# Optimization experiments

Hardware: AMD Instinct MI355X
Metric: run time of the kernel (lower is better)

Reference implementation:

```python
import jax, jax.numpy as jnp
import numpy as np

N_EMBD = 512
N_HEAD = 8
HEAD_DIM = N_EMBD // N_HEAD
MAX_REL = 5
B, T = 8, 1024  # T must be <= 2*N_EMBD due to scores[:, :, :T, :T] slice


def setup_inputs() -> dict:
    key = jax.random.key(0)
    ks = jax.random.split(key, 10)
    C, d = N_EMBD, HEAD_DIM
    s = 1.0 / np.sqrt(C)
    return {
        "x": jax.random.normal(ks[0], (B, T, C), jnp.float32),
        # nn.Linear weights are [out, in]
        "w1_w": jax.random.normal(ks[1], (C, C), jnp.float32) * s,
        "w1_b": jnp.zeros((C,), jnp.float32),
        "w2": jax.random.uniform(ks[2], (d, 2 * C), jnp.float32, -0.001, 0.001),
        "b2": jnp.zeros((2 * C,), jnp.float32),
        "v_w": jax.random.normal(ks[3], (C, C), jnp.float32) * s,
        "v_b": jnp.zeros((C,), jnp.float32),
        "proj_w": jax.random.normal(ks[4], (C, C), jnp.float32) * s,
        "proj_b": jnp.zeros((C,), jnp.float32),
        # RelativePosition embeddings table: [2*max_rel+1, head_dim]
        "rel_v_table": jax.random.normal(ks[5], (2 * MAX_REL + 1, d), jnp.float32) * s,
    }


def reference(x, w1_w, w1_b, w2, b2, v_w, v_b, proj_w, proj_b, rel_v_table):
    Bq, Tq, C = x.shape
    H, d = N_HEAD, C // N_HEAD
    # per-position MLP synthesizer scores: relu(w1(x)) [B,H,T,d] @ w2 [d,2C] + b2
    relu_out = jax.nn.relu(x @ w1_w.T + w1_b).reshape(Bq, Tq, H, d).transpose(0, 2, 1, 3)
    scores = (relu_out @ w2 + b2)[:, :, :, :Tq]  # [B,H,T,T]
    causal = jnp.tril(jnp.ones((Tq, Tq), dtype=bool))
    scores = jnp.where(causal[None, None], scores, jnp.float32(-1e10))
    prob_attn = jax.nn.softmax(scores, axis=-1)
    # standard value path
    v = (x @ v_w.T + v_b).reshape(Bq, Tq, H, d).transpose(0, 2, 1, 3)  # [B,H,T,d]
    y1 = prob_attn @ v  # [B,H,T,d]
    # relative-position value path: table lookup per (q,k) pair
    dist = jnp.arange(Tq)[None, :] - jnp.arange(Tq)[:, None]
    idx = jnp.clip(dist, -MAX_REL, 0) + MAX_REL  # [T,T] in [0, 2*MAX_REL]
    v2 = rel_v_table[idx]  # [T,T,d]
    y2 = jnp.einsum('bhqk,qkd->bhqd', prob_attn, v2)
    y = (y1 + y2).transpose(0, 2, 1, 3).reshape(Bq, Tq, C)
    return y @ proj_w.T + proj_b
```

## Files before the change

kernel.cpp:

```cpp
#include <hip/hip_runtime.h>
#include <cstdint>

#define B_ 8
#define T_ 1024
#define C_ 512
#define H_ 8

typedef __attribute__((ext_vector_type(8))) short bf16x8;
typedef __attribute__((ext_vector_type(4))) float f32x4;

__device__ __forceinline__ unsigned short f2bf(float f) {
  uint32_t u = __float_as_uint(f);
  u += 0x7FFFu + ((u >> 16) & 1u);
  return (unsigned short)(u >> 16);
}
__device__ __forceinline__ float bf2f(unsigned short h) {
  return __uint_as_float(((uint32_t)h) << 16);
}

__global__ __launch_bounds__(256) void cvt_bf16(
    const float* __restrict__ in, unsigned short* __restrict__ out, int n4) {
  int i = blockIdx.x * 256 + threadIdx.x;
  if (i < n4) {
    float4 f = reinterpret_cast<const float4*>(in)[i];
    uint2 o;
    o.x = (uint32_t)f2bf(f.x) | ((uint32_t)f2bf(f.y) << 16);
    o.y = (uint32_t)f2bf(f.z) | ((uint32_t)f2bf(f.w) << 16);
    reinterpret_cast<uint2*>(out)[i] = o;
  }
}

__global__ __launch_bounds__(256) void transpose_cvt(
    const float* __restrict__ in, unsigned short* __restrict__ out, int R, int Cc) {
  __shared__ float tile[32][33];
  const int c0 = blockIdx.x * 32, r0 = blockIdx.y * 32;
  const int t = threadIdx.x;
  {
    int ri = t >> 3, ci = (t & 7) * 4;
    float4 f = *reinterpret_cast<const float4*>(&in[(size_t)(r0 + ri) * Cc + c0 + ci]);
    tile[ri][ci] = f.x; tile[ri][ci + 1] = f.y; tile[ri][ci + 2] = f.z; tile[ri][ci + 3] = f.w;
  }
  __syncthreads();
  {
    int co = t >> 3, ro = (t & 7) * 4;
    uint2 o;
    o.x = (uint32_t)f2bf(tile[ro][co])     | ((uint32_t)f2bf(tile[ro + 1][co]) << 16);
    o.y = (uint32_t)f2bf(tile[ro + 2][co]) | ((uint32_t)f2bf(tile[ro + 3][co]) << 16);
    *reinterpret_cast<uint2*>(&out[(size_t)(c0 + co) * R + r0 + ro]) = o;
  }
}

__global__ __launch_bounds__(256) void transpose_bb(
    const unsigned short* __restrict__ in, unsigned short* __restrict__ out, int R, int Cc) {
  __shared__ unsigned short tile[32][36];
  const int c0 = blockIdx.x * 32, r0 = blockIdx.y * 32;
  const int t = threadIdx.x;
  {
    int ri = t >> 3, ci = (t & 7) * 4;
    uint2 d = *reinterpret_cast<const uint2*>(&in[(size_t)(r0 + ri) * Cc + c0 + ci]);
    *reinterpret_cast<uint2*>(&tile[ri][ci]) = d;
  }
  __syncthreads();
  {
    int co = t >> 3, ro = (t & 7) * 4;
    uint2 o;
    o.x = (uint32_t)tile[ro][co]     | ((uint32_t)tile[ro + 1][co] << 16);
    o.y = (uint32_t)tile[ro + 2][co] | ((uint32_t)tile[ro + 3][co] << 16);
    *reinterpret_cast<uint2*>(&out[(size_t)(c0 + co) * R + r0 + ro]) = o;
  }
}

template<bool RELU, bool OBF16>
__global__ __launch_bounds__(256) void gemm_mfma(
    const unsigned short* __restrict__ A, const unsigned short* __restrict__ W,
    const float* __restrict__ bias, void* __restrict__ out,
    int M, int N, int K)
{
  __shared__ unsigned short As[128 * 64];
  __shared__ unsigned short Ws[128 * 64];

  const int tid = threadIdx.x;
  const int lane = tid & 63;
  const int wid = tid >> 6;
  const int wm = wid >> 1, wn = wid & 1;
  const int m0 = blockIdx.y * 128, n0 = blockIdx.x * 128;
  const int r15 = lane & 15, g4 = lane >> 4;

  f32x4 acc[4][4] = {};

  for (int k0 = 0; k0 < K; k0 += 64) {
    __syncthreads();
    #pragma unroll
    for (int p = 0; p < 4; ++p) {
      int idx = tid + p * 256;
      int row = idx >> 3, sl = idx & 7;
      int byte = row * 128 + sl * 16;
      byte ^= ((byte >> 9) & 1) << 5;
      uint4 da = *reinterpret_cast<const uint4*>(&A[(size_t)(m0 + row) * K + k0 + sl * 8]);
      *reinterpret_cast<uint4*>(reinterpret_cast<char*>(As) + byte) = da;
      uint4 dw = *reinterpret_cast<const uint4*>(&W[(size_t)(n0 + row) * K + k0 + sl * 8]);
      *reinterpret_cast<uint4*>(reinterpret_cast<char*>(Ws) + byte) = dw;
    }
    __syncthreads();
    #pragma unroll
    for (int ks = 0; ks < 2; ++ks) {
      bf16x8 af[4], bfr[4];
      #pragma unroll
      for (int f = 0; f < 4; ++f) {
        int ab = (wm * 64 + f * 16 + r15) * 128 + ks * 64 + g4 * 16;
        ab ^= ((ab >> 9) & 1) << 5;
        af[f] = *reinterpret_cast<const bf16x8*>(reinterpret_cast<char*>(As) + ab);
        int bb = (wn * 64 + f * 16 + r15) * 128 + ks * 64 + g4 * 16;
        bb ^= ((bb >> 9) & 1) << 5;
        bfr[f] = *reinterpret_cast<const bf16x8*>(reinterpret_cast<char*>(Ws) + bb);
      }
      #pragma unroll
      for (int i = 0; i < 4; ++i)
        #pragma unroll
        for (int j = 0; j < 4; ++j)
          acc[i][j] = __builtin_amdgcn_mfma_f32_16x16x32_bf16(af[i], bfr[j], acc[i][j], 0, 0, 0);
    }
  }

  #pragma unroll
  for (int i = 0; i < 4; ++i) {
    int m = m0 + wm * 64 + i * 16 + g4 * 4;
    #pragma unroll
    for (int j = 0; j < 4; ++j) {
      int n = n0 + wn * 64 + j * 16 + r15;
      float bj = bias[n];
      #pragma unroll
      for (int rg = 0; rg < 4; ++rg) {
        float z = acc[i][j][rg] + bj;
        z = RELU ? fmaxf(z, 0.f) : z;
        if (OBF16) ((unsigned short*)out)[(size_t)(m + rg) * N + n] = f2bf(z);
        else       ((float*)out)[(size_t)(m + rg) * N + n] = z;
      }
    }
  }
}

#define SA_VLOAD(K0)                                                                  \
  do {                                                                                \
    { int c = tid;       int row = c >> 3, sl = c & 7;                                \
      w0 = *reinterpret_cast<const uint4*>(&w2t[(size_t)((K0) + row) * 64 + sl * 8]); } \
    { int c = tid + 256; int row = c >> 3, sl = c & 7;                                \
      w1 = *reinterpret_cast<const uint4*>(&w2t[(size_t)((K0) + row) * 64 + sl * 8]); } \
    { int c = tid;       int row = c >> 3, sl = c & 7;                                \
      v0 = *reinterpret_cast<const uint4*>(&vT[(size_t)(h * 64 + row) * 8192 + b * 1024 + (K0) + sl * 8]); } \
    { int c = tid + 256; int row = c >> 3, sl = c & 7;                                \
      v1 = *reinterpret_cast<const uint4*>(&vT[(size_t)(h * 64 + row) * 8192 + b * 1024 + (K0) + sl * 8]); } \
    if (tid < 16) bq = *reinterpret_cast<const float4*>(&b2[(K0) + tid * 4]);         \
  } while (0)

#define SA_VSTORE()                                                                   \
  do {                                                                                \
    { int c = tid;       int row = c >> 3, sl = c & 7;                                \
      *reinterpret_cast<uint4*>(W2 + row * 128 + ((sl ^ (row & 7)) << 4)) = w0; }     \
    { int c = tid + 256; int row = c >> 3, sl = c & 7;                                \
      *reinterpret_cast<uint4*>(W2 + row * 128 + ((sl ^ (row & 7)) << 4)) = w1; }     \
    { int c = tid;       int row = c >> 3, sl = c & 7;                                \
      *reinterpret_cast<uint4*>(Vt + row * 128 + ((sl ^ (row & 7)) << 4)) = v0; }     \
    { int c = tid + 256; int row = c >> 3, sl = c & 7;                                \
      *reinterpret_cast<uint4*>(Vt + row * 128 + ((sl ^ (row & 7)) << 4)) = v1; }     \
    if (tid < 16) *reinterpret_cast<float4*>(&b2L[tid * 4]) = bq;                     \
  } while (0)

__global__ __launch_bounds__(256) void synth_attn_mfma(
    const unsigned short* __restrict__ rb, const unsigned short* __restrict__ vT,
    const unsigned short* __restrict__ w2t, const float* __restrict__ b2,
    const float* __restrict__ table, unsigned short* __restrict__ ya)
{
  __shared__ alignas(16) unsigned short RtS[64 * 64];
  __shared__ alignas(16) unsigned short W2S[64 * 64];
  __shared__ alignas(16) unsigned short ElS[64 * 64];
  __shared__ alignas(16) unsigned short VtS[80 * 64];
  __shared__ float b2L[64];
  __shared__ float tap[64][5];
  __shared__ float tabs[6][64];

  char* Rt = (char*)RtS;
  char* W2 = (char*)W2S;
  char* El = (char*)ElS;
  char* Vt = (char*)VtS;

  const int tid = threadIdx.x;
  const int lane = tid & 63, w = tid >> 6;
  const int l15 = lane & 15, g = lane >> 4;
  const int bid = blockIdx.x;
  const int pp = bid & 7;
  const int bh = bid >> 3;
  const int b = bh >> 3, h = bh & 7;

  #pragma unroll
  for (int t2 = 0; t2 < 2; ++t2) {
    int idx = tid + t2 * 256;
    if (idx < 384) ((float*)tabs)[idx] = table[idx];
  }
  {
    int row = 64 + (tid >> 4), chunk = tid & 15;
    uint2 val;
    val.x = (row == 64) ? 0x3F803F80u : 0u;
    val.y = val.x;
    *reinterpret_cast<uint2*>(Vt + row * 128 + chunk * 8) = val;
  }

  uint4 w0, w1, v0, v1; float4 bq;

  for (int half = 0; half < 2; ++half) {
    const int qt = half ? (15 - pp) : pp;
    const int q0 = qt * 64;

    __syncthreads();
    #pragma unroll
    for (int t2 = 0; t2 < 2; ++t2) {
      int c = tid + t2 * 256; int row = c >> 3, sl = c & 7;
      uint4 d = *reinterpret_cast<const uint4*>(
          &rb[(size_t)(b * 1024 + q0 + row) * 512 + h * 64 + sl * 8]);
      *reinterpret_cast<uint4*>(Rt + row * 128 + ((sl ^ (row & 7)) << 4)) = d;
    }
    if (lane < 16) {
      int qr = w * 16 + lane;
      #pragma unroll
      for (int jj = 0; jj < 5; ++jj) tap[qr][jj] = 0.f;
    }

    f32x4 acc[4] = {};
    f32x4 accS = {};

    SA_VLOAD(0);
    for (int kt = 0; kt <= qt; ++kt) {
      const int k0 = kt * 64;
      __syncthreads();
      SA_VSTORE();
      if (kt < qt) SA_VLOAD(k0 + 64);
      __syncthreads();

      const int arow = w * 16 + l15;
      const int arx = l15 & 7;
      bf16x8 a0 = *reinterpret_cast<const bf16x8*>(Rt + arow * 128 + ((g ^ arx) << 4));
      bf16x8 a1 = *reinterpret_cast<const bf16x8*>(Rt + arow * 128 + (((4 + g) ^ arx) << 4));
      f32x4 sf[4] = {};
      #pragma unroll
      for (int j = 0; j < 4; ++j) {
        int row = 16 * j + l15, rx = row & 7;
        bf16x8 b0 = *reinterpret_cast<const bf16x8*>(W2 + row * 128 + ((g ^ rx) << 4));
        bf16x8 b1 = *reinterpret_cast<const bf16x8*>(W2 + row * 128 + (((4 + g) ^ rx) << 4));
        sf[j] = __builtin_amdgcn_mfma_f32_16x16x32_bf16(a0, b0, sf[j], 0, 0, 0);
        sf[j] = __builtin_amdgcn_mfma_f32_16x16x32_bf16(a1, b1, sf[j], 0, 0, 0);
      }

      if (kt == qt) {
        #pragma unroll
        for (int j = 0; j < 4; ++j) {
          int kc = 16 * j + l15;
          float bk = b2L[kc];
          #pragma unroll
          for (int rr = 0; rr < 4; ++rr) {
            int qr = w * 16 + g * 4 + rr;
            float ex = (kc <= qr) ? __expf(sf[j][rr] + bk) : 0.f;
            int byte = qr * 128 + ((((kc >> 3) ^ (qr & 7)) << 4) | ((kc & 7) << 1));
            *reinterpret_cast<unsigned short*>(El + byte) = f2bf(ex);
          }
        }
      } else {
        #pragma unroll
        for (int j = 0; j < 4; ++j) {
          int kc = 16 * j + l15;
          float bk = b2L[kc];
          #pragma unroll
          for (int rr = 0; rr < 4; ++rr) {
            int qr = w * 16 + g * 4 + rr;
            float ex = __expf(sf[j][rr] + bk);
            int byte = qr * 128 + ((((kc >> 3) ^ (qr & 7)) << 4) | ((kc & 7) << 1));
            *reinterpret_cast<unsigned short*>(El + byte) = f2bf(ex);
          }
        }
      }

      bf16x8 ae0 = *reinterpret_cast<const bf16x8*>(El + arow * 128 + ((g ^ arx) << 4));
      bf16x8 ae1 = *reinterpret_cast<const bf16x8*>(El + arow * 128 + (((4 + g) ^ arx) << 4));
      #pragma unroll
      for (int j = 0; j < 4; ++j) {
        int row = 16 * j + l15, rx = row & 7;
        bf16x8 vb0 = *reinterpret_cast<const bf16x8*>(Vt + row * 128 + ((g ^ rx) << 4));
        bf16x8 vb1 = *reinterpret_cast<const bf16x8*>(Vt + row * 128 + (((4 + g) ^ rx) << 4));
        acc[j] = __builtin_amdgcn_mfma_f32_16x16x32_bf16(ae0, vb0, acc[j], 0, 0, 0);
        acc[j] = __builtin_amdgcn_mfma_f32_16x16x32_bf16(ae1, vb1, acc[j], 0, 0, 0);
      }
      {
        int row = 64 + l15, rx = row & 7;
        bf16x8 o0 = *reinterpret_cast<const bf16x8*>(Vt + row * 128 + ((g ^ rx) << 4));
        bf16x8 o1 = *reinterpret_cast<const bf16x8*>(Vt + row * 128 + (((4 + g) ^ rx) << 4));
        accS = __builtin_amdgcn_mfma_f32_16x16x32_bf16(ae0, o0, accS, 0, 0, 0);
        accS = __builtin_amdgcn_mfma_f32_16x16x32_bf16(ae1, o1, accS, 0, 0, 0);
      }

      if (lane < 16) {
        int qr = w * 16 + lane;
        int off = q0 + qr - 4 - k0;
        #pragma unroll
        for (int jj = 0; jj < 5; ++jj) {
          int kk = off + jj;
          if ((unsigned)kk < 64u) {
            int byte = qr * 128 + ((((kk >> 3) ^ (qr & 7)) << 4) | ((kk & 7) << 1));
            tap[qr][jj] += bf2f(*reinterpret_cast<unsigned short*>(El + byte));
          }
        }
      }
    }

    float inv[4], tp[4][5];
    #pragma unroll
    for (int rr = 0; rr < 4; ++rr) {
      float ls = __shfl(accS[rr], lane & 48, 64);
      inv[rr] = 1.f / ls;
      int qr = w * 16 + g * 4 + rr;
      #pragma unroll
      for (int jj = 0; jj < 5; ++jj) tp[rr][jj] = tap[qr][jj] * inv[rr];
    }
    #pragma unroll
    for (int j = 0; j < 4; ++j) {
      int dd = 16 * j + l15;
      float t0 = tabs[0][dd];
      float dt[5];
      #pragma unroll
      for (int jj = 0; jj < 5; ++jj) dt[jj] = tabs[jj + 1][dd] - t0;
      #pragma unroll
      for (int rr = 0; rr < 4; ++rr) {
        int qr = w * 16 + g * 4 + rr;
        float y = acc[j][rr] * inv[rr] + t0;
        #pragma unroll
        for (int jj = 0; jj < 5; ++jj) y = fmaf(tp[rr][jj], dt[jj], y);
        ya[(size_t)(b * 1024 + q0 + qr) * 512 + h * 64 + dd] = f2bf(y);
      }
    }
  }
}

extern "C" void kernel_launch(void* const* d_in, const int* in_sizes, int n_in,
                              void* d_out, int out_size, void* d_ws, size_t ws_size,
                              hipStream_t stream) {
  const float* x      = (const float*)d_in[0];
  const float* w1_w   = (const float*)d_in[1];
  const float* w1_b   = (const float*)d_in[2];
  const float* w2     = (const float*)d_in[3];
  const float* b2     = (const float*)d_in[4];
  const float* v_w    = (const float*)d_in[5];
  const float* v_b    = (const float*)d_in[6];
  const float* proj_w = (const float*)d_in[7];
  const float* proj_b = (const float*)d_in[8];
  const float* relv   = (const float*)d_in[9];
  float* out = (float*)d_out;

  const size_t buf = (size_t)B_ * T_ * C_;
  const size_t wsz = (size_t)C_ * C_;
  unsigned short* rb    = (unsigned short*)d_ws;
  unsigned short* vbb   = rb + buf;
  unsigned short* xb    = vbb + buf;
  unsigned short* w1b   = xb + buf;
  unsigned short* vwb   = w1b + wsz;
  unsigned short* projb = vwb + wsz;
  unsigned short* w2t   = projb + wsz;
  unsigned short* vT    = xb;
  unsigned short* yab   = vbb;

  cvt_bf16<<<(int)(buf / 4 + 255) / 256, 256, 0, stream>>>(x, xb, (int)(buf / 4));
  cvt_bf16<<<(int)(wsz / 4 + 255) / 256, 256, 0, stream>>>(w1_w, w1b, (int)(wsz / 4));
  cvt_bf16<<<(int)(wsz / 4 + 255) / 256, 256, 0, stream>>>(v_w, vwb, (int)(wsz / 4));
  cvt_bf16<<<(int)(wsz / 4 + 255) / 256, 256, 0, stream>>>(proj_w, projb, (int)(wsz / 4));
  transpose_cvt<<<dim3(32, 2), 256, 0, stream>>>(w2, w2t, 64, 1024);

  dim3 g(C_ / 128, (B_ * T_) / 128);
  gemm_mfma<true,  true ><<<g, 256, 0, stream>>>(xb, w1b, w1_b, rb,  B_ * T_, C_, C_);
  gemm_mfma<false, true ><<<g, 256, 0, stream>>>(xb, vwb, v_b,  vbb, B_ * T_, C_, C_);
  transpose_bb<<<dim3(16, 256), 256, 0, stream>>>(vbb, vT, 8192, 512);

  synth_attn_mfma<<<512, 256, 0, stream>>>(rb, vT, w2t, b2, relv, yab);

  gemm_mfma<false, false><<<g, 256, 0, stream>>>(yab, projb, proj_b, out, B_ * T_, C_, C_);
}
```

Baseline: 171.5 us.

## Fuse w1/v GEMMs with transposed V output, use direct-to-LDS loads

Merges the w1 and v projections into one GEMM kernel that shares the x tile and writes V directly in transposed layout, which removes the separate transpose kernel and one read of x. The three weight conversions are merged into one launch. The GEMMs switch to 64x128 tiles so more blocks are launched, and they use global_load_lds to fill shared memory directly. The LDS XOR swizzle is dropped, which may add bank conflicts, and the transposed V stores are narrow 8-byte writes with a large stride.

```diff
diff --git a/kernel.cpp b/kernel.cpp
--- a/kernel.cpp
+++ b/kernel.cpp
@@ -16,6 +16,12 @@
 }
 __device__ __forceinline__ float bf2f(unsigned short h) {
   return __uint_as_float(((uint32_t)h) << 16);
+}
+
+__device__ __forceinline__ void gload16(const void* g, void* lds) {
+  __builtin_amdgcn_global_load_lds(
+      (const __attribute__((address_space(1))) void*)g,
+      (__attribute__((address_space(3))) void*)lds, 16, 0, 0);
 }
 
 __global__ __launch_bounds__(256) void cvt_bf16(
@@ -30,6 +36,21 @@
   }
 }
 
+__global__ __launch_bounds__(256) void cvt_w3(
+    const float* __restrict__ w1, const float* __restrict__ vw,
+    const float* __restrict__ pw, unsigned short* __restrict__ w1b,
+    unsigned short* __restrict__ vwb, unsigned short* __restrict__ pjb) {
+  int seg = blockIdx.x >> 8;
+  int i = (blockIdx.x & 255) * 256 + threadIdx.x;
+  const float* in = (seg == 0) ? w1 : (seg == 1) ? vw : pw;
+  unsigned short* o = (seg == 0) ? w1b : (seg == 1) ? vwb : pjb;
+  float4 f = reinterpret_cast<const float4*>(in)[i];
+  uint2 u;
+  u.x = (uint32_t)f2bf(f.x) | ((uint32_t)f2bf(f.y) << 16);
+  u.y = (uint32_t)f2bf(f.z) | ((uint32_t)f2bf(f.w) << 16);
+  reinterpret_cast<uint2*>(o)[i] = u;
+}
+
 __global__ __launch_bounds__(256) void transpose_cvt(
     const float* __restrict__ in, unsigned short* __restrict__ out, int R, int Cc) {
   __shared__ float tile[32][33];
@@ -50,92 +71,153 @@
   }
 }
 
-__global__ __launch_bounds__(256) void transpose_bb(
-    const unsigned short* __restrict__ in, unsigned short* __restrict__ out, int R, int Cc) {
-  __shared__ unsigned short tile[32][36];
-  const int c0 = blockIdx.x * 32, r0 = blockIdx.y * 32;
-  const int t = threadIdx.x;
-  {
-    int ri = t >> 3, ci = (t & 7) * 4;
-    uint2 d = *reinterpret_cast<const uint2*>(&in[(size_t)(r0 + ri) * Cc + c0 + ci]);
-    *reinterpret_cast<uint2*>(&tile[ri][ci]) = d;
-  }
-  __syncthreads();
-  {
-    int co = t >> 3, ro = (t & 7) * 4;
-    uint2 o;
-    o.x = (uint32_t)tile[ro][co]     | ((uint32_t)tile[ro + 1][co] << 16);
-    o.y = (uint32_t)tile[ro + 2][co] | ((uint32_t)tile[ro + 3][co] << 16);
-    *reinterpret_cast<uint2*>(&out[(size_t)(c0 + co) * R + r0 + ro]) = o;
-  }
-}
-
-template<bool RELU, bool OBF16>
-__global__ __launch_bounds__(256) void gemm_mfma(
-    const unsigned short* __restrict__ A, const unsigned short* __restrict__ W,
-    const float* __restrict__ bias, void* __restrict__ out,
-    int M, int N, int K)
+__global__ __launch_bounds__(256) void gemm_w1v(
+    const unsigned short* __restrict__ xb,
+    const unsigned short* __restrict__ w1b, const unsigned short* __restrict__ vwb,
+    const float* __restrict__ w1_bias, const float* __restrict__ v_bias,
+    unsigned short* __restrict__ rb, unsigned short* __restrict__ vT)
 {
-  __shared__ unsigned short As[128 * 64];
-  __shared__ unsigned short Ws[128 * 64];
+  __shared__ alignas(16) unsigned short Xs[64 * 64];
+  __shared__ alignas(16) unsigned short W1s[128 * 64];
+  __shared__ alignas(16) unsigned short Vs[128 * 64];
 
   const int tid = threadIdx.x;
-  const int lane = tid & 63;
-  const int wid = tid >> 6;
-  const int wm = wid >> 1, wn = wid & 1;
-  const int m0 = blockIdx.y * 128, n0 = blockIdx.x * 128;
-  const int r15 = lane & 15, g4 = lane >> 4;
-
-  f32x4 acc[4][4] = {};
-
-  for (int k0 = 0; k0 < K; k0 += 64) {
+  const int lane = tid & 63, w = tid >> 6;
+  const int l15 = lane & 15, g4 = lane >> 4;
+  const int wr = w >> 1, wc = w & 1;
+  const int n0 = blockIdx.x * 128;
+  const int m0 = blockIdx.y * 64;
+  const int lrow = lane >> 3;
+  const int lcol = (lane & 7) * 8;
+
+  f32x4 a1[2][4] = {};
+  f32x4 a2[2][4] = {};
+
+  for (int k0 = 0; k0 < 512; k0 += 64) {
     __syncthreads();
     #pragma unroll
-    for (int p = 0; p < 4; ++p) {
-      int idx = tid + p * 256;
-      int row = idx >> 3, sl = idx & 7;
-      int byte = row * 128 + sl * 16;
-      byte ^= ((byte >> 9) & 1) << 5;
-      uint4 da = *reinterpret_cast<const uint4*>(&A[(size_t)(m0 + row) * K + k0 + sl * 8]);
-      *reinterpret_cast<uint4*>(reinterpret_cast<char*>(As) + byte) = da;
-      uint4 dw = *reinterpret_cast<const uint4*>(&W[(size_t)(n0 + row) * K + k0 + sl * 8]);
-      *reinterpret_cast<uint4*>(reinterpret_cast<char*>(Ws) + byte) = dw;
+    for (int cc = 0; cc < 10; ++cc) {
+      int c = w * 10 + cc;
+      if (c < 8) {
+        gload16(&xb[(size_t)(m0 + c * 8 + lrow) * 512 + k0 + lcol],
+                (char*)Xs + c * 1024);
+      } else if (c < 24) {
+        int cl = c - 8;
+        gload16(&w1b[(size_t)(n0 + cl * 8 + lrow) * 512 + k0 + lcol],
+                (char*)W1s + cl * 1024);
+      } else {
+        int cl = c - 24;
+        gload16(&vwb[(size_t)(n0 + cl * 8 + lrow) * 512 + k0 + lcol],
+                (char*)Vs + cl * 1024);
+      }
     }
     __syncthreads();
+
     #pragma unroll
     for (int ks = 0; ks < 2; ++ks) {
-      bf16x8 af[4], bfr[4];
-      #pragma unroll
-      for (int f = 0; f < 4; ++f) {
-        int ab = (wm * 64 + f * 16 + r15) * 128 + ks * 64 + g4 * 16;
-        ab ^= ((ab >> 9) & 1) << 5;
-        af[f] = *reinterpret_cast<const bf16x8*>(reinterpret_cast<char*>(As) + ab);
-        int bb = (wn * 64 + f * 16 + r15) * 128 + ks * 64 + g4 * 16;
-        bb ^= ((bb >> 9) & 1) << 5;
-        bfr[f] = *reinterpret_cast<const bf16x8*>(reinterpret_cast<char*>(Ws) + bb);
-      }
-      #pragma unroll
-      for (int i = 0; i < 4; ++i)
+      bf16x8 af[2], wf[4], vf[4];
+      #pragma unroll
+      for (int i = 0; i < 2; ++i)
+        af[i] = *(const bf16x8*)((const char*)Xs +
+                 (wr * 32 + 16 * i + l15) * 128 + ks * 64 + g4 * 16);
+      #pragma unroll
+      for (int j = 0; j < 4; ++j) {
+        int n = wc * 64 + 16 * j + l15;
+        wf[j] = *(const bf16x8*)((const char*)W1s + n * 128 + ks * 64 + g4 * 16);
+        vf[j] = *(const bf16x8*)((const char*)Vs  + n * 128 + ks * 64 + g4 * 16);
+      }
+      #pragma unroll
+      for (int i = 0; i < 2; ++i)
+        #pragma unroll
+        for (int j = 0; j < 4; ++j) {
+          a1[i][j] = __builtin_amdgcn_mfma_f32_16x16x32_bf16(af[i], wf[j], a1[i][j], 0, 0, 0);
+          a2[i][j] = __builtin_amdgcn_mfma_f32_16x16x32_bf16(af[i], vf[j], a2[i][j], 0, 0, 0);
+        }
+    }
+  }
+
+  #pragma unroll
+  for (int i = 0; i < 2; ++i) {
+    int mb = m0 + wr * 32 + 16 * i + g4 * 4;
+    #pragma unroll
+    for (int j = 0; j < 4; ++j) {
+      int n = n0 + wc * 64 + 16 * j + l15;
+      float b1 = w1_bias[n];
+      #pragma unroll
+      for (int rg = 0; rg < 4; ++rg)
+        rb[(size_t)(mb + rg) * 512 + n] = f2bf(fmaxf(a1[i][j][rg] + b1, 0.f));
+      float bv = v_bias[n];
+      unsigned short p[4];
+      #pragma unroll
+      for (int rg = 0; rg < 4; ++rg) p[rg] = f2bf(a2[i][j][rg] + bv);
+      *reinterpret_cast<uint2*>(&vT[(size_t)n * 8192 + mb]) =
+          *reinterpret_cast<const uint2*>(p);
+    }
+  }
+}
+
+__global__ __launch_bounds__(256) void gemm_proj(
+    const unsigned short* __restrict__ A, const unsigned short* __restrict__ Wb,
+    const float* __restrict__ bias, float* __restrict__ out)
+{
+  __shared__ alignas(16) unsigned short As[64 * 64];
+  __shared__ alignas(16) unsigned short Ws[128 * 64];
+
+  const int tid = threadIdx.x;
+  const int lane = tid & 63, w = tid >> 6;
+  const int l15 = lane & 15, g4 = lane >> 4;
+  const int wr = w >> 1, wc = w & 1;
+  const int n0 = blockIdx.x * 128;
+  const int m0 = blockIdx.y * 64;
+  const int lrow = lane >> 3, lcol = (lane & 7) * 8;
+
+  f32x4 acc[2][4] = {};
+
+  for (int k0 = 0; k0 < 512; k0 += 64) {
+    __syncthreads();
+    #pragma unroll
+    for (int cc = 0; cc < 6; ++cc) {
+      int c = w * 6 + cc;
+      if (c < 8) {
+        gload16(&A[(size_t)(m0 + c * 8 + lrow) * 512 + k0 + lcol],
+                (char*)As + c * 1024);
+      } else {
+        int cl = c - 8;
+        gload16(&Wb[(size_t)(n0 + cl * 8 + lrow) * 512 + k0 + lcol],
+                (char*)Ws + cl * 1024);
+      }
+    }
+    __syncthreads();
+
+    #pragma unroll
+    for (int ks = 0; ks < 2; ++ks) {
+      bf16x8 af[2], wf[4];
+      #pragma unroll
+      for (int i = 0; i < 2; ++i)
+        af[i] = *(const bf16x8*)((const char*)As +
+                 (wr * 32 + 16 * i + l15) * 128 + ks * 64 + g4 * 16);
+      #pragma unroll
+      for (int j = 0; j < 4; ++j)
+        wf[j] = *(const bf16x8*)((const char*)Ws +
+                 (wc * 64 + 16 * j + l15) * 128 + ks * 64 + g4 * 16);
+      #pragma unroll
+      for (int i = 0; i < 2; ++i)
         #pragma unroll
         for (int j = 0; j < 4; ++j)
-          acc[i][j] = __builtin_amdgcn_mfma_f32_16x16x32_bf16(af[i], bfr[j], acc[i][j], 0, 0, 0);
+          acc[i][j] = __builtin_amdgcn_mfma_f32_16x16x32_bf16(af[i], wf[j], acc[i][j], 0, 0, 0);
     }
   }
 
   #pragma unroll
-  for (int i = 0; i < 4; ++i) {
-    int m = m0 + wm * 64 + i * 16 + g4 * 4;
+  for (int i = 0; i < 2; ++i) {
+    int mb = m0 + wr * 32 + 16 * i + g4 * 4;
     #pragma unroll
     for (int j = 0; j < 4; ++j) {
-      int n = n0 + wn * 64 + j * 16 + r15;
+      int n = n0 + wc * 64 + 16 * j + l15;
       float bj = bias[n];
       #pragma unroll
-      for (int rg = 0; rg < 4; ++rg) {
-        float z = acc[i][j][rg] + bj;
-        z = RELU ? fmaxf(z, 0.f) : z;
-        if (OBF16) ((unsigned short*)out)[(size_t)(m + rg) * N + n] = f2bf(z);
-        else       ((float*)out)[(size_t)(m + rg) * N + n] = z;
-      }
+      for (int rg = 0; rg < 4; ++rg)
+        out[(size_t)(mb + rg) * 512 + n] = acc[i][j][rg] + bj;
     }
   }
 }
@@ -356,27 +438,21 @@
   const size_t buf = (size_t)B_ * T_ * C_;
   const size_t wsz = (size_t)C_ * C_;
   unsigned short* rb    = (unsigned short*)d_ws;
-  unsigned short* vbb   = rb + buf;
-  unsigned short* xb    = vbb + buf;
-  unsigned short* w1b   = xb + buf;
+  unsigned short* vT    = rb + buf;
+  unsigned short* xb    = vT + buf;
+  unsigned short* yab   = xb + buf;
+  unsigned short* w1b   = yab + buf;
   unsigned short* vwb   = w1b + wsz;
   unsigned short* projb = vwb + wsz;
   unsigned short* w2t   = projb + wsz;
-  unsigned short* vT    = xb;
-  unsigned short* yab   = vbb;
 
   cvt_bf16<<<(int)(buf / 4 + 255) / 256, 256, 0, stream>>>(x, xb, (int)(buf / 4));
-  cvt_bf16<<<(int)(wsz / 4 + 255) / 256, 256, 0, stream>>>(w1_w, w1b, (int)(wsz / 4));
-  cvt_bf16<<<(int)(wsz / 4 + 255) / 256, 256, 0, stream>>>(v_w, vwb, (int)(wsz / 4));
-  cvt_bf16<<<(int)(wsz / 4 + 255) / 256, 256, 0, stream>>>(proj_w, projb, (int)(wsz / 4));
+  cvt_w3<<<768, 256, 0, stream>>>(w1_w, v_w, proj_w, w1b, vwb, projb);
   transpose_cvt<<<dim3(32, 2), 256, 0, stream>>>(w2, w2t, 64, 1024);
 
-  dim3 g(C_ / 128, (B_ * T_) / 128);
-  gemm_mfma<true,  true ><<<g, 256, 0, stream>>>(xb, w1b, w1_b, rb,  B_ * T_, C_, C_);
-  gemm_mfma<false, true ><<<g, 256, 0, stream>>>(xb, vwb, v_b,  vbb, B_ * T_, C_, C_);
-  transpose_bb<<<dim3(16, 256), 256, 0, stream>>>(vbb, vT, 8192, 512);
+  gemm_w1v<<<dim3(4, 128), 256, 0, stream>>>(xb, w1b, vwb, w1_b, v_b, rb, vT);
 
   synth_attn_mfma<<<512, 256, 0, stream>>>(rb, vT, w2t, b2, relv, yab);
 
-  gemm_mfma<false, false><<<g, 256, 0, stream>>>(yab, projb, proj_b, out, B_ * T_, C_, C_);
-}
+  gemm_proj<<<dim3(4, 128), 256, 0, stream>>>(yab, projb, proj_b, out);
+}
```

After: 150.7 us. -12.1%, faster.
